# Kernel optimization log

Measured on AMD Instinct MI355X. Metric: run time of the kernel, lower is better.

## Reference

```python
import jax, jax.numpy as jnp
import numpy as np

DECAY = 0.8
COMMITMENT = 1.0
EPS = 1e-05


def setup_inputs() -> dict:
    key = jax.random.key(0)
    k1, k2 = jax.random.split(key)
    x = jax.random.normal(k1, (8, 4096, 256), dtype=jnp.float32)
    embed = jax.random.normal(k2, (8192, 256), dtype=jnp.float32)
    cluster_size = jnp.zeros((8192,), dtype=jnp.float32)
    embed_avg = embed  # torch registers embed_avg = embed.clone()
    return {"x": x, "embed": embed, "cluster_size": cluster_size, "embed_avg": embed_avg}


def reference(x, embed, cluster_size, embed_avg):
    # EuclideanCodebook.forward (training mode) + VectorQuantize straight-through.
    K, D = embed.shape
    shape = x.shape
    flatten = x.reshape(-1, D)  # [T, D], T = B*N

    dist = (2.0 * (flatten @ embed.T)
            - jnp.sum(flatten * flatten, axis=-1, keepdims=True)
            - jnp.sum(embed * embed, axis=-1)[None, :])  # [T, K]
    embed_ind = jnp.argmax(dist, axis=-1)  # [T]

    quantize = embed[embed_ind].reshape(shape)  # gather

    # EMA codebook statistics (scatter-add instead of materializing one-hot [T,K])
    bins = jax.ops.segment_sum(jnp.ones_like(embed_ind, dtype=x.dtype), embed_ind, num_segments=K)  # [K]
    embed_sum = jax.ops.segment_sum(flatten, embed_ind, num_segments=K)  # [K, D]

    new_cluster_size = cluster_size * DECAY + (1.0 - DECAY) * bins
    new_embed_avg = embed_avg * DECAY + (1.0 - DECAY) * embed_sum

    total = new_cluster_size.sum()
    smoothed = (new_cluster_size + EPS) / (total + K * EPS) * total  # laplace smoothing
    new_embed = new_embed_avg / smoothed[:, None]

    commit_loss = jnp.mean((jax.lax.stop_gradient(quantize) - x) ** 2) * COMMITMENT
    quantize_st = x + jax.lax.stop_gradient(quantize - x)  # straight-through

    ind_out = embed_ind.reshape(shape[:-1])
    return quantize_st, ind_out, commit_loss, new_embed, new_cluster_size, new_embed_avg
```

## Files before the change

kernel.cpp:

```cpp
#include <hip/hip_runtime.h>

#define DECAYF 0.8f
#define OMDF   0.2f
#define EPSF   1e-5f
#define COMMITF 1.0f
#define MARGINF 0.024f
#define FIXCAP  8192
#define MAXR    64

typedef _Float16 h8v __attribute__((ext_vector_type(8)));
typedef float f4v __attribute__((ext_vector_type(4)));

__device__ inline void gload_lds16(const void* g, void* l) {
  __builtin_amdgcn_global_load_lds(
      (const __attribute__((address_space(1))) unsigned int*)g,
      (__attribute__((address_space(3))) unsigned int*)l, 16, 0, 0);
}

__global__ __launch_bounds__(256) void k_pre(
    const float* __restrict__ embed, char* __restrict__ Ews,
    float* __restrict__ zero_p, int zero_n, float* __restrict__ ee, int K, int D)
{
  const int tid = threadIdx.x;
  const int gid0 = blockIdx.x * 256 + tid;
  const int gstride = gridDim.x * 256;

  for (int i = gid0; i < zero_n; i += gstride) zero_p[i] = 0.0f;

  for (int gid = gid0; gid < K * (D / 8); gid += gstride) {
    int k = gid >> 5;
    int d0 = (gid & 31) * 8;
    const float* ep = embed + (size_t)k * D + d0;
    float4 v0 = *(const float4*)(ep);
    float4 v1 = *(const float4*)(ep + 4);
    float f[8] = {v0.x, v0.y, v0.z, v0.w, v1.x, v1.y, v1.z, v1.w};
    h8v h;
#pragma unroll
    for (int e = 0; e < 8; ++e) h[e] = (_Float16)f[e];
    int tt = k >> 6;
    int c = k & 63;
    int byteoff = c * 512 + ((d0 * 2) ^ ((c & 7) << 4));
    *(h8v*)(Ews + (size_t)tt * 32768 + byteoff) = h;
  }

  {
    int wave = tid >> 6;
    int lane = tid & 63;
    int k = blockIdx.x * 4 + wave;
    if (k < K) {
      const float* e = embed + (size_t)k * D;
      float s = 0.f;
      for (int d = lane * 4; d < D; d += 256) {
        float4 v = *reinterpret_cast<const float4*>(e + d);
        s += v.x * v.x + v.y * v.y + v.z * v.z + v.w * v.w;
      }
      for (int off = 32; off > 0; off >>= 1) s += __shfl_down(s, off);
      if (lane == 0) ee[k] = 0.5f * s;
    }
  }
}

__device__ __forceinline__ void upd2(float s, int code, float& b1, float& b2, int& bi) {
  if (s > b1) { b2 = b1; b1 = s; bi = code; }
  else if (s > b2) { b2 = s; }
}

__device__ __forceinline__ void k_body(
    int TT, int NT, char* lds, const char* Ews, const float* ee,
    int w, int lane, int ch, int l15, int rowbyte0,
    const int (&dbyte)[8],
    const h8v (&xh)[2][8],
    f4v (&CUR)[2][2], f4v (&PRV)[2][2],
    float EEP0, float EEP1, float& EEC0, float& EEC1,
    float (&best)[2][4], float (&bst2)[2][4], int (&bidx)[2][4])
{
  const int k0 = TT * 64;
  const char* cb = lds + (TT & 1) * 32768;
  if (TT + 1 < NT) {
    const char* src = Ews + (size_t)(TT + 1) * 32768 + w * 8192 + lane * 16;
    char* dst = lds + ((TT + 1) & 1) * 32768 + w * 8192;
#pragma unroll
    for (int q = 0; q < 8; ++q) gload_lds16(src + q * 1024, dst + q * 1024);
  }
  EEC0 = ee[k0 + ch * 32 + l15];
  EEC1 = ee[k0 + ch * 32 + l15 + 16];
  const int c0p = k0 - 64 + ch * 32 + l15;
  const int c1p = c0p + 16;
#pragma unroll
  for (int rf = 0; rf < 2; ++rf) {
    CUR[rf][0] = (f4v){0.f, 0.f, 0.f, 0.f};
    CUR[rf][1] = (f4v){0.f, 0.f, 0.f, 0.f};
  }
  h8v Bh0[2], Bh1[2];
  {
    const char* p = cb + rowbyte0 + dbyte[0];
    Bh0[0] = *(const h8v*)(p);
    Bh1[0] = *(const h8v*)(p + 8192);
  }
#pragma unroll
  for (int ks = 0; ks < 8; ++ks) {
    const int cs = ks & 1, ns = cs ^ 1;
    if (ks < 7) {
      const char* p = cb + rowbyte0 + dbyte[ks + 1];
      Bh0[ns] = *(const h8v*)(p);
      Bh1[ns] = *(const h8v*)(p + 8192);
    }
    __builtin_amdgcn_s_setprio(1);
    CUR[0][0] = __builtin_amdgcn_mfma_f32_16x16x32_f16(xh[0][ks], Bh0[cs], CUR[0][0], 0, 0, 0);
    CUR[0][1] = __builtin_amdgcn_mfma_f32_16x16x32_f16(xh[0][ks], Bh1[cs], CUR[0][1], 0, 0, 0);
    CUR[1][0] = __builtin_amdgcn_mfma_f32_16x16x32_f16(xh[1][ks], Bh0[cs], CUR[1][0], 0, 0, 0);
    CUR[1][1] = __builtin_amdgcn_mfma_f32_16x16x32_f16(xh[1][ks], Bh1[cs], CUR[1][1], 0, 0, 0);
    __builtin_amdgcn_s_setprio(0);
    {
      const int rf = ks >> 2, ii = ks & 3;
      upd2(PRV[rf][0][ii] - EEP0, c0p, best[rf][ii], bst2[rf][ii], bidx[rf][ii]);
      upd2(PRV[rf][1][ii] - EEP1, c1p, best[rf][ii], bst2[rf][ii], bidx[rf][ii]);
    }
  }
  __syncthreads();
}

__global__ __launch_bounds__(256, 2) void k_dist(
    const float* __restrict__ x, const char* __restrict__ Ews,
    const float* __restrict__ ee, float* __restrict__ ind_f,
    int* __restrict__ idx_out, int* __restrict__ wl, int* __restrict__ cnt,
    int T, int K)
{
  extern __shared__ char lds[];
  const int tid = threadIdx.x;
  const int w = tid >> 6, lane = tid & 63;
  const int l15 = lane & 15, lk = lane >> 4;
  const int rgrp = w >> 1, ch = w & 1;
  const int row0 = blockIdx.x * 64 + rgrp * 32;
  const int NT = K / 64;

  h8v xh[2][8];
#pragma unroll
  for (int rf = 0; rf < 2; ++rf) {
    const float* xp = x + (size_t)(row0 + rf * 16 + l15) * 256 + lk * 8;
#pragma unroll
    for (int ks = 0; ks < 8; ++ks) {
      float4 v0 = *(const float4*)(xp + ks * 32);
      float4 v1 = *(const float4*)(xp + ks * 32 + 4);
      float f[8] = {v0.x, v0.y, v0.z, v0.w, v1.x, v1.y, v1.z, v1.w};
      h8v h;
#pragma unroll
      for (int e = 0; e < 8; ++e) h[e] = (_Float16)f[e];
      xh[rf][ks] = h;
    }
  }

  float best[2][4], bst2[2][4];
  int bidx[2][4];
#pragma unroll
  for (int rf = 0; rf < 2; ++rf)
#pragma unroll
    for (int i = 0; i < 4; ++i) { best[rf][i] = -3.0e38f; bst2[rf][i] = -3.0e38f; bidx[rf][i] = 0; }

  const int swz = (l15 & 7) << 4;
  const int rowbyte0 = (ch * 32 + l15) * 512;
  int dbyte[8];
#pragma unroll
  for (int ks = 0; ks < 8; ++ks) dbyte[ks] = (ks * 64 + lk * 16) ^ swz;

  {
    const char* src = Ews + (size_t)w * 8192 + lane * 16;
    char* dst = lds + w * 8192;
#pragma unroll
    for (int q = 0; q < 8; ++q)
      gload_lds16(src + q * 1024, dst + q * 1024);
  }
  __syncthreads();

  f4v accA[2][2], accB[2][2];
#pragma unroll
  for (int rf = 0; rf < 2; ++rf) {
    accB[rf][0] = (f4v){-3.0e38f, -3.0e38f, -3.0e38f, -3.0e38f};
    accB[rf][1] = (f4v){-3.0e38f, -3.0e38f, -3.0e38f, -3.0e38f};
  }
  float eeX0 = 0.f, eeX1 = 0.f, eeY0 = 0.f, eeY1 = 0.f;

  for (int tt = 0; tt < NT; tt += 2) {
    k_body(tt,     NT, lds, Ews, ee, w, lane, ch, l15, rowbyte0, dbyte, xh,
           accA, accB, eeX0, eeX1, eeY0, eeY1, best, bst2, bidx);
    k_body(tt + 1, NT, lds, Ews, ee, w, lane, ch, l15, rowbyte0, dbyte, xh,
           accB, accA, eeY0, eeY1, eeX0, eeX1, best, bst2, bidx);
  }
  {
    const int c0 = (NT - 1) * 64 + ch * 32 + l15, c1 = c0 + 16;
#pragma unroll
    for (int rf = 0; rf < 2; ++rf)
#pragma unroll
      for (int ii = 0; ii < 4; ++ii) {
        upd2(accB[rf][0][ii] - eeX0, c0, best[rf][ii], bst2[rf][ii], bidx[rf][ii]);
        upd2(accB[rf][1][ii] - eeX1, c1, best[rf][ii], bst2[rf][ii], bidx[rf][ii]);
      }
  }

#pragma unroll
  for (int rf = 0; rf < 2; ++rf)
#pragma unroll
    for (int i = 0; i < 4; ++i) {
      float s = best[rf][i], s2 = bst2[rf][i];
      int mi = bidx[rf][i];
#pragma unroll
      for (int off = 1; off < 16; off <<= 1) {
        float os = __shfl_xor(s, off);
        float os2 = __shfl_xor(s2, off);
        int oi = __shfl_xor(mi, off);
        if (os > s || (os == s && oi < mi)) {
          s2 = fmaxf(s, os2);
          s = os; mi = oi;
        } else {
          s2 = fmaxf(s2, os);
        }
      }
      best[rf][i] = s; bst2[rf][i] = s2; bidx[rf][i] = mi;
    }

  float* S  = (float*)lds;
  float* S2 = S + 128;
  int*   MI = (int*)(S2 + 128);
  if (l15 == 0) {
#pragma unroll
    for (int rf = 0; rf < 2; ++rf)
#pragma unroll
      for (int i = 0; i < 4; ++i) {
        int rl = rf * 16 + lk * 4 + i;
        int a = rgrp * 64 + ch * 32 + rl;
        S[a]  = best[rf][i];
        S2[a] = bst2[rf][i];
        MI[a] = bidx[rf][i];
      }
  }
  __syncthreads();
  if (ch == 0 && lane < 32) {
    int a0 = rgrp * 64 + lane;
    float sA = S[a0],      s2A = S2[a0];      int miA = MI[a0];
    float sB = S[a0 + 32], s2B = S2[a0 + 32]; int miB = MI[a0 + 32];
    float s, s2; int mi;
    if (sB > sA || (sB == sA && miB < miA)) { s = sB; mi = miB; s2 = fmaxf(sA, s2B); }
    else                                    { s = sA; mi = miA; s2 = fmaxf(s2A, sB); }
    int row = row0 + lane;
    idx_out[row] = mi;
    ind_f[row] = (float)mi;
    if (s - s2 < MARGINF) {
      int slot = atomicAdd(cnt, 1);
      if (slot < FIXCAP) wl[slot] = row;
    }
  }
}

__global__ __launch_bounds__(256) void k_fix1(
    const float* __restrict__ x, const float* __restrict__ embed,
    const float* __restrict__ ee, const int* __restrict__ wl,
    const int* __restrict__ cnt, float* __restrict__ pval,
    int* __restrict__ pidx)
{
  __shared__ float Xs[8][256];
  const int b = blockIdx.x & 255;
  const int g = blockIdx.x >> 8;
  const int t = threadIdx.x;
  int n = *cnt; if (n > FIXCAP) n = FIXCAP;
  const int c = b * 32 + (t & 31);
  const float* er = embed + (size_t)c * 256;
  const float eec = ee[c];
  const int rl = t >> 5;

  for (int r0 = g * 8; r0 < n; r0 += 32) {
    __syncthreads();
    for (int i = t; i < 8 * 64; i += 256) {
      int rr = i >> 6, dq = i & 63;
      int wi = r0 + rr; if (wi >= n) wi = n - 1;
      int row = wl[wi];
      ((float4*)Xs[rr])[dq] = *(const float4*)(x + (size_t)row * 256 + dq * 4);
    }
    __syncthreads();
    const float* xr = Xs[rl];
    float s0 = 0.f, s1 = 0.f, s2a = 0.f, s3 = 0.f;
#pragma unroll
    for (int d = 0; d < 256; d += 16) {
      float4 e0 = *(const float4*)(er + d);
      float4 e1 = *(const float4*)(er + d + 4);
      float4 e2 = *(const float4*)(er + d + 8);
      float4 e3 = *(const float4*)(er + d + 12);
      s0 = fmaf(xr[d + 0], e0.x, s0);  s0 = fmaf(xr[d + 1], e0.y, s0);
      s0 = fmaf(xr[d + 2], e0.z, s0);  s0 = fmaf(xr[d + 3], e0.w, s0);
      s1 = fmaf(xr[d + 4], e1.x, s1);  s1 = fmaf(xr[d + 5], e1.y, s1);
      s1 = fmaf(xr[d + 6], e1.z, s1);  s1 = fmaf(xr[d + 7], e1.w, s1);
      s2a = fmaf(xr[d + 8], e2.x, s2a);  s2a = fmaf(xr[d + 9], e2.y, s2a);
      s2a = fmaf(xr[d + 10], e2.z, s2a); s2a = fmaf(xr[d + 11], e2.w, s2a);
      s3 = fmaf(xr[d + 12], e3.x, s3);  s3 = fmaf(xr[d + 13], e3.y, s3);
      s3 = fmaf(xr[d + 14], e3.z, s3);  s3 = fmaf(xr[d + 15], e3.w, s3);
    }
    float s = ((s0 + s1) + (s2a + s3)) - eec;
    int mi = c;
#pragma unroll
    for (int off = 1; off < 32; off <<= 1) {
      float os = __shfl_xor(s, off);
      int oi = __shfl_xor(mi, off);
      if (os > s || (os == s && oi < mi)) { s = os; mi = oi; }
    }
    int wi = r0 + rl;
    if ((t & 31) == 0 && wi < n) {
      pval[(size_t)wi * 256 + b] = s;
      pidx[(size_t)wi * 256 + b] = mi;
    }
  }
}

__global__ __launch_bounds__(256) void k_fix2(
    const int* __restrict__ wl, const int* __restrict__ cnt,
    const float* __restrict__ pval, const int* __restrict__ pidx,
    float* __restrict__ ind_f, int* __restrict__ idx_out)
{
  __shared__ float bv[256];
  __shared__ int bi[256];
  const int t = threadIdx.x;
  int n = *cnt; if (n > FIXCAP) n = FIXCAP;
  for (int it = blockIdx.x; it < n; it += gridDim.x) {
    __syncthreads();
    bv[t] = pval[(size_t)it * 256 + t];
    bi[t] = pidx[(size_t)it * 256 + t];
    __syncthreads();
    for (int sh = 128; sh > 0; sh >>= 1) {
      if (t < sh) {
        if (bv[t + sh] > bv[t] || (bv[t + sh] == bv[t] && bi[t + sh] < bi[t])) {
          bv[t] = bv[t + sh]; bi[t] = bi[t + sh];
        }
      }
      __syncthreads();
    }
    if (t == 0) {
      int row = wl[it];
      idx_out[row] = bi[0];
      ind_f[row] = (float)bi[0];
    }
  }
}

__global__ __launch_bounds__(256) void k_cnt(
    const int* __restrict__ idx, int* __restrict__ cntr, int* __restrict__ rlist,
    int* __restrict__ olist, int* __restrict__ ocnt, int T)
{
  int r = blockIdx.x * 256 + threadIdx.x;
  if (r >= T) return;
  int k = idx[r];
  int slot = atomicAdd(&cntr[k], 1);
  if (slot < MAXR) rlist[k * MAXR + slot] = r;
  else { int o = atomicAdd(ocnt, 1); olist[o] = r; }
}

__global__ __launch_bounds__(256) void k_ovf(
    const float* __restrict__ x, const int* __restrict__ idx,
    const int* __restrict__ olist, const int* __restrict__ ocnt,
    float* __restrict__ ovfsum)
{
  int wave = threadIdx.x >> 6, lane = threadIdx.x & 63;
  int n = *ocnt;
  for (int i = blockIdx.x * 4 + wave; i < n; i += gridDim.x * 4) {
    int row = olist[i];
    int k = idx[row];
    int d0 = lane * 4;
    float4 xv = *(const float4*)(x + (size_t)row * 256 + d0);
    atomicAdd(&ovfsum[(size_t)k * 256 + d0 + 0], xv.x);
    atomicAdd(&ovfsum[(size_t)k * 256 + d0 + 1], xv.y);
    atomicAdd(&ovfsum[(size_t)k * 256 + d0 + 2], xv.z);
    atomicAdd(&ovfsum[(size_t)k * 256 + d0 + 3], xv.w);
  }
}

__global__ void k_gather(const float* __restrict__ x, const float* __restrict__ embed,
                         const int* __restrict__ idx, float* __restrict__ quant,
                         float* __restrict__ lslots, int T, int D)
{
  int wave = threadIdx.x >> 6;
  int lane = threadIdx.x & 63;
  int row = blockIdx.x * 4 + wave;
  if (row >= T) return;
  int k = idx[row];
  const float* xr = x + (size_t)row * D;
  const float* er = embed + (size_t)k * D;
  float* qr = quant + (size_t)row * D;
  float lsum = 0.f;
  for (int d = lane * 4; d < D; d += 256) {
    float4 xv = *reinterpret_cast<const float4*>(xr + d);
    float4 ev = *reinterpret_cast<const float4*>(er + d);
    *reinterpret_cast<float4*>(qr + d) = ev;
    float dx = ev.x - xv.x, dy = ev.y - xv.y, dz = ev.z - xv.z, dw = ev.w - xv.w;
    lsum += dx * dx + dy * dy + dz * dz + dw * dw;
  }
  for (int off = 32; off > 0; off >>= 1) lsum += __shfl_down(lsum, off);
  if (lane == 0) atomicAdd(&lslots[row & 255], lsum);
}

__global__ void k_ema1(const float* __restrict__ cs, const int* __restrict__ cntr,
                       float* __restrict__ ncs, float* __restrict__ total_acc, int K)
{
  int k = blockIdx.x * 256 + threadIdx.x;
  float v = 0.f;
  if (k < K) {
    v = cs[k] * DECAYF + OMDF * (float)cntr[k];
    ncs[k] = v;
  }
  for (int off = 32; off > 0; off >>= 1) v += __shfl_down(v, off);
  __shared__ float s4[4];
  if ((threadIdx.x & 63) == 0) s4[threadIdx.x >> 6] = v;
  __syncthreads();
  if (threadIdx.x == 0) atomicAdd(total_acc, s4[0] + s4[1] + s4[2] + s4[3]);
}

__global__ __launch_bounds__(256) void k_ema2(
    const float* __restrict__ x, const float* __restrict__ ea,
    const int* __restrict__ cntr, const int* __restrict__ rlist,
    const float* __restrict__ ovfsum, const float* __restrict__ ncs,
    const float* __restrict__ total_acc, float* __restrict__ ne,
    float* __restrict__ nea, int K, int D)
{
  int wave = threadIdx.x >> 6, lane = threadIdx.x & 63;
  int k = blockIdx.x * 4 + wave;
  if (k >= K) return;
  int c = cntr[k];
  int m = c < MAXR ? c : MAXR;
  int d0 = lane * 4;
  float4 s = *(const float4*)(ovfsum + (size_t)k * 256 + d0);
  for (int i = 0; i < m; ++i) {
    int r = rlist[k * MAXR + i];
    float4 xv = *(const float4*)(x + (size_t)r * 256 + d0);
    s.x += xv.x; s.y += xv.y; s.z += xv.z; s.w += xv.w;
  }
  float4 eav = *(const float4*)(ea + (size_t)k * 256 + d0);
  float total = *total_acc;
  float csk = ncs[k];
  float sm = (csk + EPSF) / (total + (float)K * EPSF) * total;
  float rs = 1.0f / sm;
  float v0 = eav.x * DECAYF + OMDF * s.x;
  float v1 = eav.y * DECAYF + OMDF * s.y;
  float v2 = eav.z * DECAYF + OMDF * s.z;
  float v3 = eav.w * DECAYF + OMDF * s.w;
  size_t o = (size_t)k * 256 + d0;
  nea[o + 0] = v0; nea[o + 1] = v1; nea[o + 2] = v2; nea[o + 3] = v3;
  ne[o + 0] = v0 * rs; ne[o + 1] = v1 * rs; ne[o + 2] = v2 * rs; ne[o + 3] = v3 * rs;
}

__global__ void k_loss(const float* __restrict__ lslots, float* __restrict__ out_loss,
                       float scale)
{
  int tid = threadIdx.x;
  float v = lslots[tid];
  for (int off = 32; off > 0; off >>= 1) v += __shfl_down(v, off);
  __shared__ float s4[4];
  if ((tid & 63) == 0) s4[tid >> 6] = v;
  __syncthreads();
  if (tid == 0) out_loss[0] = (s4[0] + s4[1] + s4[2] + s4[3]) * scale;
}

extern "C" void kernel_launch(void* const* d_in, const int* in_sizes, int n_in,
                              void* d_out, int out_size, void* d_ws, size_t ws_size,
                              hipStream_t stream)
{
  const float* x     = (const float*)d_in[0];
  const float* embed = (const float*)d_in[1];
  const float* cs    = (const float*)d_in[2];
  const float* ea    = (const float*)d_in[3];
  const int K = in_sizes[2];
  const int D = in_sizes[1] / K;
  const int T = in_sizes[0] / D;

  float* out   = (float*)d_out;
  float* o_q   = out;
  float* o_ind = out + (size_t)T * D;
  float* o_ls  = o_ind + T;
  float* o_ne  = o_ls + 1;
  float* o_ncs = o_ne + (size_t)K * D;
  float* o_nea = o_ncs + K;

  float* w      = (float*)d_ws;
  float* ee     = w;
  int*   idx    = (int*)(w + K);
  int*   wl     = idx + T;
  float* pval   = (float*)(wl + FIXCAP);
  int*   pidx   = (int*)(pval + (size_t)FIXCAP * 256);
  int*   rlist  = pidx + (size_t)FIXCAP * 256;
  int*   olist  = rlist + (size_t)K * MAXR;
  float* ovfsum = (float*)(olist + T);
  float* lslots = ovfsum + (size_t)K * D;
  float* total  = lslots + 256;
  int*   cnt    = (int*)(total + 1);
  int*   cntr   = cnt + 1;
  int*   ocnt   = cntr + K;
  int zero_n = K * D + 256 + 1 + 1 + K + 1;
  size_t ews_off = (((size_t)(ocnt + 1 - (int*)w)) + 63) & ~(size_t)63;
  char* Ews = (char*)(w + ews_off);

  k_pre<<<2048, 256, 0, stream>>>(embed, Ews, ovfsum, zero_n, ee, K, D);
  k_dist<<<T / 64, 256, 65536, stream>>>(x, Ews, ee, o_ind, idx, wl, cnt, T, K);
  k_fix1<<<1024, 256, 0, stream>>>(x, embed, ee, wl, cnt, pval, pidx);
  k_fix2<<<1024, 256, 0, stream>>>(wl, cnt, pval, pidx, o_ind, idx);
  k_cnt<<<(T + 255) / 256, 256, 0, stream>>>(idx, cntr, rlist, olist, ocnt, T);
  k_ovf<<<128, 256, 0, stream>>>(x, idx, olist, ocnt, ovfsum);
  k_gather<<<(T + 3) / 4, 256, 0, stream>>>(x, embed, idx, o_q, lslots, T, D);
  k_ema1<<<(K + 255) / 256, 256, 0, stream>>>(cs, cntr, o_ncs, total, K);
  k_ema2<<<(K + 3) / 4, 256, 0, stream>>>(x, ea, cntr, rlist, ovfsum, o_ncs, total,
                                          o_ne, o_nea, K, D);
  k_loss<<<1, 256, 0, stream>>>(lslots, o_ls, COMMITF / ((float)T * (float)D));
}
```

Measured before the change: 467.0 us.

## Give each wave all 64 rows and a 16-code slice per tile

Each wave in the distance kernel now covers all 64 rows of the block against its own 16 codewords per tile. Before, waves were split into two row groups of 32 rows, each handling 32 codes. This cuts LDS B-fragment reads per MFMA, since one B load now feeds four MFMAs instead of two loads feeding four. In exchange, each wave holds twice as many x fragments and best/second-best trackers in registers, which may pressure occupancy under launch_bounds(256,2). The final cross-wave reduction now merges four partial results per row, with ties no longer broken by the lower index.

```diff
diff --git a/kernel.cpp b/kernel.cpp
--- a/kernel.cpp
+++ b/kernel.cpp
@@ -67,12 +67,12 @@
 
 __device__ __forceinline__ void k_body(
     int TT, int NT, char* lds, const char* Ews, const float* ee,
-    int w, int lane, int ch, int l15, int rowbyte0,
+    int w, int lane, int l15, int rowbyte0,
     const int (&dbyte)[8],
-    const h8v (&xh)[2][8],
-    f4v (&CUR)[2][2], f4v (&PRV)[2][2],
-    float EEP0, float EEP1, float& EEC0, float& EEC1,
-    float (&best)[2][4], float (&bst2)[2][4], int (&bidx)[2][4])
+    const h8v (&xh)[4][8],
+    f4v (&CUR)[4], f4v (&PRV)[4],
+    float EEP, float& EEC,
+    float (&best)[4][4], float (&bst2)[4][4], int (&bidx)[4][4])
 {
   const int k0 = TT * 64;
   const char* cb = lds + (TT & 1) * 32768;
@@ -82,39 +82,28 @@
 #pragma unroll
     for (int q = 0; q < 8; ++q) gload_lds16(src + q * 1024, dst + q * 1024);
   }
-  EEC0 = ee[k0 + ch * 32 + l15];
-  EEC1 = ee[k0 + ch * 32 + l15 + 16];
-  const int c0p = k0 - 64 + ch * 32 + l15;
-  const int c1p = c0p + 16;
-#pragma unroll
-  for (int rf = 0; rf < 2; ++rf) {
-    CUR[rf][0] = (f4v){0.f, 0.f, 0.f, 0.f};
-    CUR[rf][1] = (f4v){0.f, 0.f, 0.f, 0.f};
-  }
-  h8v Bh0[2], Bh1[2];
-  {
-    const char* p = cb + rowbyte0 + dbyte[0];
-    Bh0[0] = *(const h8v*)(p);
-    Bh1[0] = *(const h8v*)(p + 8192);
-  }
+  EEC = ee[k0 + w * 16 + l15];
+  const int cp = k0 - 64 + w * 16 + l15;
+#pragma unroll
+  for (int rf = 0; rf < 4; ++rf) CUR[rf] = (f4v){0.f, 0.f, 0.f, 0.f};
+  h8v B[2];
+  B[0] = *(const h8v*)(cb + rowbyte0 + dbyte[0]);
 #pragma unroll
   for (int ks = 0; ks < 8; ++ks) {
     const int cs = ks & 1, ns = cs ^ 1;
-    if (ks < 7) {
-      const char* p = cb + rowbyte0 + dbyte[ks + 1];
-      Bh0[ns] = *(const h8v*)(p);
-      Bh1[ns] = *(const h8v*)(p + 8192);
-    }
+    if (ks < 7) B[ns] = *(const h8v*)(cb + rowbyte0 + dbyte[ks + 1]);
     __builtin_amdgcn_s_setprio(1);
-    CUR[0][0] = __builtin_amdgcn_mfma_f32_16x16x32_f16(xh[0][ks], Bh0[cs], CUR[0][0], 0, 0, 0);
-    CUR[0][1] = __builtin_amdgcn_mfma_f32_16x16x32_f16(xh[0][ks], Bh1[cs], CUR[0][1], 0, 0, 0);
-    CUR[1][0] = __builtin_amdgcn_mfma_f32_16x16x32_f16(xh[1][ks], Bh0[cs], CUR[1][0], 0, 0, 0);
-    CUR[1][1] = __builtin_amdgcn_mfma_f32_16x16x32_f16(xh[1][ks], Bh1[cs], CUR[1][1], 0, 0, 0);
+    CUR[0] = __builtin_amdgcn_mfma_f32_16x16x32_f16(xh[0][ks], B[cs], CUR[0], 0, 0, 0);
+    CUR[1] = __builtin_amdgcn_mfma_f32_16x16x32_f16(xh[1][ks], B[cs], CUR[1], 0, 0, 0);
+    CUR[2] = __builtin_amdgcn_mfma_f32_16x16x32_f16(xh[2][ks], B[cs], CUR[2], 0, 0, 0);
+    CUR[3] = __builtin_amdgcn_mfma_f32_16x16x32_f16(xh[3][ks], B[cs], CUR[3], 0, 0, 0);
     __builtin_amdgcn_s_setprio(0);
     {
-      const int rf = ks >> 2, ii = ks & 3;
-      upd2(PRV[rf][0][ii] - EEP0, c0p, best[rf][ii], bst2[rf][ii], bidx[rf][ii]);
-      upd2(PRV[rf][1][ii] - EEP1, c1p, best[rf][ii], bst2[rf][ii], bidx[rf][ii]);
+      const int s0 = 2 * ks, s1 = 2 * ks + 1;
+      const int rf0 = s0 >> 2, ii0 = s0 & 3;
+      const int rf1 = s1 >> 2, ii1 = s1 & 3;
+      upd2(PRV[rf0][ii0] - EEP, cp, best[rf0][ii0], bst2[rf0][ii0], bidx[rf0][ii0]);
+      upd2(PRV[rf1][ii1] - EEP, cp, best[rf1][ii1], bst2[rf1][ii1], bidx[rf1][ii1]);
     }
   }
   __syncthreads();
@@ -130,13 +119,12 @@
   const int tid = threadIdx.x;
   const int w = tid >> 6, lane = tid & 63;
   const int l15 = lane & 15, lk = lane >> 4;
-  const int rgrp = w >> 1, ch = w & 1;
-  const int row0 = blockIdx.x * 64 + rgrp * 32;
+  const int row0 = blockIdx.x * 64;
   const int NT = K / 64;
 
-  h8v xh[2][8];
-#pragma unroll
-  for (int rf = 0; rf < 2; ++rf) {
+  h8v xh[4][8];
+#pragma unroll
+  for (int rf = 0; rf < 4; ++rf) {
     const float* xp = x + (size_t)(row0 + rf * 16 + l15) * 256 + lk * 8;
 #pragma unroll
     for (int ks = 0; ks < 8; ++ks) {
@@ -150,15 +138,15 @@
     }
   }
 
-  float best[2][4], bst2[2][4];
-  int bidx[2][4];
-#pragma unroll
-  for (int rf = 0; rf < 2; ++rf)
+  float best[4][4], bst2[4][4];
+  int bidx[4][4];
+#pragma unroll
+  for (int rf = 0; rf < 4; ++rf)
 #pragma unroll
     for (int i = 0; i < 4; ++i) { best[rf][i] = -3.0e38f; bst2[rf][i] = -3.0e38f; bidx[rf][i] = 0; }
 
   const int swz = (l15 & 7) << 4;
-  const int rowbyte0 = (ch * 32 + l15) * 512;
+  const int rowbyte0 = (w * 16 + l15) * 512;
   int dbyte[8];
 #pragma unroll
   for (int ks = 0; ks < 8; ++ks) dbyte[ks] = (ks * 64 + lk * 16) ^ swz;
@@ -172,33 +160,29 @@
   }
   __syncthreads();
 
-  f4v accA[2][2], accB[2][2];
-#pragma unroll
-  for (int rf = 0; rf < 2; ++rf) {
-    accB[rf][0] = (f4v){-3.0e38f, -3.0e38f, -3.0e38f, -3.0e38f};
-    accB[rf][1] = (f4v){-3.0e38f, -3.0e38f, -3.0e38f, -3.0e38f};
-  }
-  float eeX0 = 0.f, eeX1 = 0.f, eeY0 = 0.f, eeY1 = 0.f;
+  f4v accA[4], accB[4];
+#pragma unroll
+  for (int rf = 0; rf < 4; ++rf)
+    accB[rf] = (f4v){-3.0e38f, -3.0e38f, -3.0e38f, -3.0e38f};
+  float eeX = 0.f, eeY = 0.f;
 
   for (int tt = 0; tt < NT; tt += 2) {
-    k_body(tt,     NT, lds, Ews, ee, w, lane, ch, l15, rowbyte0, dbyte, xh,
-           accA, accB, eeX0, eeX1, eeY0, eeY1, best, bst2, bidx);
-    k_body(tt + 1, NT, lds, Ews, ee, w, lane, ch, l15, rowbyte0, dbyte, xh,
-           accB, accA, eeY0, eeY1, eeX0, eeX1, best, bst2, bidx);
+    k_body(tt,     NT, lds, Ews, ee, w, lane, l15, rowbyte0, dbyte, xh,
+           accA, accB, eeX, eeY, best, bst2, bidx);
+    k_body(tt + 1, NT, lds, Ews, ee, w, lane, l15, rowbyte0, dbyte, xh,
+           accB, accA, eeY, eeX, best, bst2, bidx);
   }
   {
-    const int c0 = (NT - 1) * 64 + ch * 32 + l15, c1 = c0 + 16;
-#pragma unroll
-    for (int rf = 0; rf < 2; ++rf)
-#pragma unroll
-      for (int ii = 0; ii < 4; ++ii) {
-        upd2(accB[rf][0][ii] - eeX0, c0, best[rf][ii], bst2[rf][ii], bidx[rf][ii]);
-        upd2(accB[rf][1][ii] - eeX1, c1, best[rf][ii], bst2[rf][ii], bidx[rf][ii]);
-      }
-  }
-
-#pragma unroll
-  for (int rf = 0; rf < 2; ++rf)
+    const int cp = (NT - 1) * 64 + w * 16 + l15;
+#pragma unroll
+    for (int rf = 0; rf < 4; ++rf)
+#pragma unroll
+      for (int ii = 0; ii < 4; ++ii)
+        upd2(accB[rf][ii] - eeX, cp, best[rf][ii], bst2[rf][ii], bidx[rf][ii]);
+  }
+
+#pragma unroll
+  for (int rf = 0; rf < 4; ++rf)
 #pragma unroll
     for (int i = 0; i < 4; ++i) {
       float s = best[rf][i], s2 = bst2[rf][i];
@@ -219,29 +203,33 @@
     }
 
   float* S  = (float*)lds;
-  float* S2 = S + 128;
-  int*   MI = (int*)(S2 + 128);
+  float* S2 = S + 256;
+  int*   MI = (int*)(S2 + 256);
   if (l15 == 0) {
 #pragma unroll
-    for (int rf = 0; rf < 2; ++rf)
+    for (int rf = 0; rf < 4; ++rf)
 #pragma unroll
       for (int i = 0; i < 4; ++i) {
         int rl = rf * 16 + lk * 4 + i;
-        int a = rgrp * 64 + ch * 32 + rl;
+        int a = w * 64 + rl;
         S[a]  = best[rf][i];
         S2[a] = bst2[rf][i];
         MI[a] = bidx[rf][i];
       }
   }
   __syncthreads();
-  if (ch == 0 && lane < 32) {
-    int a0 = rgrp * 64 + lane;
-    float sA = S[a0],      s2A = S2[a0];      int miA = MI[a0];
-    float sB = S[a0 + 32], s2B = S2[a0 + 32]; int miB = MI[a0 + 32];
-    float s, s2; int mi;
-    if (sB > sA || (sB == sA && miB < miA)) { s = sB; mi = miB; s2 = fmaxf(sA, s2B); }
-    else                                    { s = sA; mi = miA; s2 = fmaxf(s2A, sB); }
-    int row = row0 + lane;
+  if (w == 0) {
+    int r = lane;
+    float s = S[r], s2 = S2[r];
+    int mi = MI[r];
+#pragma unroll
+    for (int q = 1; q < 4; ++q) {
+      float sq = S[q * 64 + r], s2q = S2[q * 64 + r];
+      int miq = MI[q * 64 + r];
+      if (sq > s) { s2 = fmaxf(s, s2q); s = sq; mi = miq; }
+      else        { s2 = fmaxf(s2, sq); }
+    }
+    int row = row0 + r;
     idx_out[row] = mi;
     ind_f[row] = (float)mi;
     if (s - s2 < MARGINF) {
```

Result: slower. 476.7 us (+2.1%).

## Fuse codeword bucketing into distance/fix kernels and merge small tail kernels

Applied to the files above, without the earlier changes.

Codeword-to-row bucketing (cluster counts and row lists) now happens directly where each row's final index is decided: in the distance kernel for unambiguous rows and in the fix kernel for near-tie rows. This removes the separate counting kernel and its re-read of indices. Overflow accumulation, the cluster-size EMA and the loss reduction are merged into one small kernel, and the codeword squared norms are computed inside the fp16 conversion loop with a shuffle reduction. Together this cuts launches and a redundant pass over the codebook, at the cost of more atomics in the tail of the distance kernel.

```diff
diff --git a/kernel.cpp b/kernel.cpp
--- a/kernel.cpp
+++ b/kernel.cpp
@@ -35,28 +35,19 @@
     float4 v1 = *(const float4*)(ep + 4);
     float f[8] = {v0.x, v0.y, v0.z, v0.w, v1.x, v1.y, v1.z, v1.w};
     h8v h;
-#pragma unroll
-    for (int e = 0; e < 8; ++e) h[e] = (_Float16)f[e];
+    float ss = 0.f;
+#pragma unroll
+    for (int e = 0; e < 8; ++e) {
+      h[e] = (_Float16)f[e];
+      ss = fmaf(f[e], f[e], ss);
+    }
     int tt = k >> 6;
     int c = k & 63;
     int byteoff = c * 512 + ((d0 * 2) ^ ((c & 7) << 4));
     *(h8v*)(Ews + (size_t)tt * 32768 + byteoff) = h;
-  }
-
-  {
-    int wave = tid >> 6;
-    int lane = tid & 63;
-    int k = blockIdx.x * 4 + wave;
-    if (k < K) {
-      const float* e = embed + (size_t)k * D;
-      float s = 0.f;
-      for (int d = lane * 4; d < D; d += 256) {
-        float4 v = *reinterpret_cast<const float4*>(e + d);
-        s += v.x * v.x + v.y * v.y + v.z * v.z + v.w * v.w;
-      }
-      for (int off = 32; off > 0; off >>= 1) s += __shfl_down(s, off);
-      if (lane == 0) ee[k] = 0.5f * s;
-    }
+#pragma unroll
+    for (int off = 1; off < 32; off <<= 1) ss += __shfl_xor(ss, off);
+    if ((gid & 31) == 0) ee[k] = 0.5f * ss;
   }
 }
 
@@ -124,6 +115,8 @@
     const float* __restrict__ x, const char* __restrict__ Ews,
     const float* __restrict__ ee, float* __restrict__ ind_f,
     int* __restrict__ idx_out, int* __restrict__ wl, int* __restrict__ cnt,
+    int* __restrict__ cntr, int* __restrict__ rlist,
+    int* __restrict__ olist, int* __restrict__ ocnt,
     int T, int K)
 {
   extern __shared__ char lds[];
@@ -244,9 +237,15 @@
     int row = row0 + lane;
     idx_out[row] = mi;
     ind_f[row] = (float)mi;
+    int flagged = 0;
     if (s - s2 < MARGINF) {
       int slot = atomicAdd(cnt, 1);
-      if (slot < FIXCAP) wl[slot] = row;
+      if (slot < FIXCAP) { wl[slot] = row; flagged = 1; }
+    }
+    if (!flagged) {
+      int slot2 = atomicAdd(&cntr[mi], 1);
+      if (slot2 < MAXR) rlist[mi * MAXR + slot2] = row;
+      else { int o = atomicAdd(ocnt, 1); olist[o] = row; }
     }
   }
 }
@@ -312,7 +311,9 @@
 __global__ __launch_bounds__(256) void k_fix2(
     const int* __restrict__ wl, const int* __restrict__ cnt,
     const float* __restrict__ pval, const int* __restrict__ pidx,
-    float* __restrict__ ind_f, int* __restrict__ idx_out)
+    float* __restrict__ ind_f, int* __restrict__ idx_out,
+    int* __restrict__ cntr, int* __restrict__ rlist,
+    int* __restrict__ olist, int* __restrict__ ocnt)
 {
   __shared__ float bv[256];
   __shared__ int bi[256];
@@ -333,40 +334,13 @@
     }
     if (t == 0) {
       int row = wl[it];
-      idx_out[row] = bi[0];
-      ind_f[row] = (float)bi[0];
-    }
-  }
-}
-
-__global__ __launch_bounds__(256) void k_cnt(
-    const int* __restrict__ idx, int* __restrict__ cntr, int* __restrict__ rlist,
-    int* __restrict__ olist, int* __restrict__ ocnt, int T)
-{
-  int r = blockIdx.x * 256 + threadIdx.x;
-  if (r >= T) return;
-  int k = idx[r];
-  int slot = atomicAdd(&cntr[k], 1);
-  if (slot < MAXR) rlist[k * MAXR + slot] = r;
-  else { int o = atomicAdd(ocnt, 1); olist[o] = r; }
-}
-
-__global__ __launch_bounds__(256) void k_ovf(
-    const float* __restrict__ x, const int* __restrict__ idx,
-    const int* __restrict__ olist, const int* __restrict__ ocnt,
-    float* __restrict__ ovfsum)
-{
-  int wave = threadIdx.x >> 6, lane = threadIdx.x & 63;
-  int n = *ocnt;
-  for (int i = blockIdx.x * 4 + wave; i < n; i += gridDim.x * 4) {
-    int row = olist[i];
-    int k = idx[row];
-    int d0 = lane * 4;
-    float4 xv = *(const float4*)(x + (size_t)row * 256 + d0);
-    atomicAdd(&ovfsum[(size_t)k * 256 + d0 + 0], xv.x);
-    atomicAdd(&ovfsum[(size_t)k * 256 + d0 + 1], xv.y);
-    atomicAdd(&ovfsum[(size_t)k * 256 + d0 + 2], xv.z);
-    atomicAdd(&ovfsum[(size_t)k * 256 + d0 + 3], xv.w);
+      int kf = bi[0];
+      idx_out[row] = kf;
+      ind_f[row] = (float)kf;
+      int slot = atomicAdd(&cntr[kf], 1);
+      if (slot < MAXR) rlist[kf * MAXR + slot] = row;
+      else { int o = atomicAdd(ocnt, 1); olist[o] = row; }
+    }
   }
 }
 
@@ -394,20 +368,44 @@
   if (lane == 0) atomicAdd(&lslots[row & 255], lsum);
 }
 
-__global__ void k_ema1(const float* __restrict__ cs, const int* __restrict__ cntr,
-                       float* __restrict__ ncs, float* __restrict__ total_acc, int K)
-{
-  int k = blockIdx.x * 256 + threadIdx.x;
-  float v = 0.f;
-  if (k < K) {
-    v = cs[k] * DECAYF + OMDF * (float)cntr[k];
-    ncs[k] = v;
-  }
+__global__ __launch_bounds__(256) void k_mid(
+    const float* __restrict__ cs, const int* __restrict__ cntr,
+    float* __restrict__ ncs, float* __restrict__ total_acc,
+    const float* __restrict__ lslots, float* __restrict__ out_loss, float scale,
+    const float* __restrict__ x, const int* __restrict__ idx,
+    const int* __restrict__ olist, const int* __restrict__ ocnt,
+    float* __restrict__ ovfsum, int K)
+{
+  const int tid = threadIdx.x;
+  const int wave = tid >> 6, lane = tid & 63;
+  if (blockIdx.x == 32) {
+    float v = lslots[tid];
+    for (int off = 32; off > 0; off >>= 1) v += __shfl_down(v, off);
+    __shared__ float s4[4];
+    if ((tid & 63) == 0) s4[tid >> 6] = v;
+    __syncthreads();
+    if (tid == 0) out_loss[0] = (s4[0] + s4[1] + s4[2] + s4[3]) * scale;
+    return;
+  }
+  int k = blockIdx.x * 256 + tid;
+  float v = cs[k] * DECAYF + OMDF * (float)cntr[k];
+  ncs[k] = v;
   for (int off = 32; off > 0; off >>= 1) v += __shfl_down(v, off);
   __shared__ float s4[4];
-  if ((threadIdx.x & 63) == 0) s4[threadIdx.x >> 6] = v;
+  if ((tid & 63) == 0) s4[tid >> 6] = v;
   __syncthreads();
-  if (threadIdx.x == 0) atomicAdd(total_acc, s4[0] + s4[1] + s4[2] + s4[3]);
+  if (tid == 0) atomicAdd(total_acc, s4[0] + s4[1] + s4[2] + s4[3]);
+  int n = *ocnt;
+  for (int i = blockIdx.x * 4 + wave; i < n; i += 128) {
+    int row = olist[i];
+    int kk = idx[row];
+    int d0 = lane * 4;
+    float4 xv = *(const float4*)(x + (size_t)row * 256 + d0);
+    atomicAdd(&ovfsum[(size_t)kk * 256 + d0 + 0], xv.x);
+    atomicAdd(&ovfsum[(size_t)kk * 256 + d0 + 1], xv.y);
+    atomicAdd(&ovfsum[(size_t)kk * 256 + d0 + 2], xv.z);
+    atomicAdd(&ovfsum[(size_t)kk * 256 + d0 + 3], xv.w);
+  }
 }
 
 __global__ __launch_bounds__(256) void k_ema2(
@@ -441,18 +439,6 @@
   size_t o = (size_t)k * 256 + d0;
   nea[o + 0] = v0; nea[o + 1] = v1; nea[o + 2] = v2; nea[o + 3] = v3;
   ne[o + 0] = v0 * rs; ne[o + 1] = v1 * rs; ne[o + 2] = v2 * rs; ne[o + 3] = v3 * rs;
-}
-
-__global__ void k_loss(const float* __restrict__ lslots, float* __restrict__ out_loss,
-                       float scale)
-{
-  int tid = threadIdx.x;
-  float v = lslots[tid];
-  for (int off = 32; off > 0; off >>= 1) v += __shfl_down(v, off);
-  __shared__ float s4[4];
-  if ((tid & 63) == 0) s4[tid >> 6] = v;
-  __syncthreads();
-  if (tid == 0) out_loss[0] = (s4[0] + s4[1] + s4[2] + s4[3]) * scale;
 }
 
 extern "C" void kernel_launch(void* const* d_in, const int* in_sizes, int n_in,
@@ -494,14 +480,15 @@
   char* Ews = (char*)(w + ews_off);
 
   k_pre<<<2048, 256, 0, stream>>>(embed, Ews, ovfsum, zero_n, ee, K, D);
-  k_dist<<<T / 64, 256, 65536, stream>>>(x, Ews, ee, o_ind, idx, wl, cnt, T, K);
+  k_dist<<<T / 64, 256, 65536, stream>>>(x, Ews, ee, o_ind, idx, wl, cnt,
+                                         cntr, rlist, olist, ocnt, T, K);
   k_fix1<<<1024, 256, 0, stream>>>(x, embed, ee, wl, cnt, pval, pidx);
-  k_fix2<<<1024, 256, 0, stream>>>(wl, cnt, pval, pidx, o_ind, idx);
-  k_cnt<<<(T + 255) / 256, 256, 0, stream>>>(idx, cntr, rlist, olist, ocnt, T);
-  k_ovf<<<128, 256, 0, stream>>>(x, idx, olist, ocnt, ovfsum);
+  k_fix2<<<1024, 256, 0, stream>>>(wl, cnt, pval, pidx, o_ind, idx,
+                                   cntr, rlist, olist, ocnt);
   k_gather<<<(T + 3) / 4, 256, 0, stream>>>(x, embed, idx, o_q, lslots, T, D);
-  k_ema1<<<(K + 255) / 256, 256, 0, stream>>>(cs, cntr, o_ncs, total, K);
+  k_mid<<<33, 256, 0, stream>>>(cs, cntr, o_ncs, total, lslots, o_ls,
+                                COMMITF / ((float)T * (float)D),
+                                x, idx, olist, ocnt, ovfsum, K);
   k_ema2<<<(K + 3) / 4, 256, 0, stream>>>(x, ea, cntr, rlist, ovfsum, o_ncs, total,
                                           o_ne, o_nea, K, D);
-  k_loss<<<1, 256, 0, stream>>>(lslots, o_ls, COMMITF / ((float)T * (float)D));
-}
+}
```

Result: no change. 462.3 us (-1.0%).
